# Optimization experiments

Measured on AMD Instinct MI355X. Metric: run time of the kernel, lower is better.

## Reference

```python
import jax, jax.numpy as jnp
import numpy as np

B, N, D, H = 8, 1024, 1024, 16
HD = D // H  # head_size = 64


def setup_inputs() -> dict:
    key = jax.random.key(0)
    k0, k1, k2, k3, k4 = jax.random.split(key, 5)
    scale = 1.0 / np.sqrt(D)
    return {
        "x": jax.random.normal(k0, (B, N, D), dtype=jnp.float32),
        "Wqkv": jax.random.normal(k1, (D, 3 * D), dtype=jnp.float32) * scale,
        "bqkv": jnp.zeros((3 * D,), dtype=jnp.float32),
        "Wo": jax.random.normal(k2, (D, D), dtype=jnp.float32) * scale,
        "bo": jnp.zeros((D,), dtype=jnp.float32),
    }


def reference(x, Wqkv, bqkv, Wo, bo):
    # Fused QKV projection: [B, N, 3D]
    qkv = jnp.einsum("bnd,de->bne", x, Wqkv) + bqkv
    q, k, v = jnp.split(qkv, 3, axis=-1)

    def split_heads(t):  # [B, N, D] -> [B, H, N, HD]
        return t.reshape(B, N, H, HD).transpose(0, 2, 1, 3)

    q, k, v = split_heads(q), split_heads(k), split_heads(v)

    # Scaled dot-product attention (no mask, dropout=0)
    scores = jnp.einsum("bhqd,bhkd->bhqk", q, k) / jnp.sqrt(jnp.float32(HD))
    alpha = jax.nn.softmax(scores, axis=-1)
    ctx = jnp.einsum("bhqk,bhkd->bhqd", alpha, v)  # [B, H, N, HD]

    ctx = ctx.transpose(0, 2, 1, 3).reshape(B, N, D)
    out = jnp.einsum("bnd,de->bne", ctx, Wo) + bo
    return out
```

## Files before the change

kernel.cpp:

```cpp
#include <hip/hip_runtime.h>
#include <cstdint>
#include <cstddef>

typedef _Float16 half_t;
typedef __attribute__((ext_vector_type(4))) _Float16 half4v;
typedef __attribute__((ext_vector_type(8))) _Float16 half8v;
typedef __attribute__((ext_vector_type(4))) float float4v;
typedef __attribute__((ext_vector_type(16))) float float16v;
typedef __attribute__((ext_vector_type(4))) unsigned uint4v;
typedef __attribute__((ext_vector_type(2))) int int2v;

typedef __attribute__((address_space(1))) const void gv_t;
typedef __attribute__((address_space(3))) void lv_t;

__device__ __forceinline__ void lds_cp16(const void* g, void* l) {
  __builtin_amdgcn_global_load_lds((gv_t*)g, (lv_t*)l, 16, 0, 0);
}

__device__ __forceinline__ unsigned pkh(float a, float b) {
  return __builtin_bit_cast(unsigned, __builtin_amdgcn_cvt_pkrtz(a, b));
}

__global__ __launch_bounds__(256) void k_cvt(const float* __restrict__ in,
                                             half_t* __restrict__ out) {
  int i = blockIdx.x * 256 + threadIdx.x;
  float4 v = ((const float4*)in)[i];
  half4v h = {(half_t)v.x, (half_t)v.y, (half_t)v.z, (half_t)v.w};
  ((half4v*)out)[i] = h;
}

__global__ __launch_bounds__(256) void k_tcvt(const float* __restrict__ in,
                                              half_t* __restrict__ out, int R, int C) {
  __shared__ float t[32][33];
  int c0 = blockIdx.x * 32, r0 = blockIdx.y * 32;
  int tc = threadIdx.x & 31, tr = threadIdx.x >> 5;
#pragma unroll
  for (int i = 0; i < 4; i++)
    t[tr + i * 8][tc] = in[(size_t)(r0 + tr + i * 8) * C + c0 + tc];
  __syncthreads();
#pragma unroll
  for (int i = 0; i < 4; i++)
    out[(size_t)(c0 + tr + i * 8) * R + r0 + tc] = (half_t)t[tc][tr + i * 8];
}

template <int EPI>
__global__ __launch_bounds__(256) void k_gemm(
    const half_t* __restrict__ A, const half_t* __restrict__ Bt,
    const float* __restrict__ bias, float* __restrict__ Cout,
    half_t* __restrict__ Qo, half_t* __restrict__ Ko, half_t* __restrict__ Vo,
    int M, int N, int K) {
  __shared__ half_t As[2][128 * 32];
  __shared__ half_t Bs[2][128 * 32];
  const int tid = threadIdx.x;
  const int lane = tid & 63;
  const int w = tid >> 6;
  const int xcd = blockIdx.x & 7;
  const int l = blockIdx.x >> 3;
  const int nc = l >> 6, r = l & 63;
  const int m0 = (xcd * 8 + (r >> 3)) * 128;
  const int n0 = (nc * 8 + (r & 7)) * 128;
  const int wr = w >> 1, wc = w & 1;

  const int c0 = w * 2, c1 = c0 + 1;
  const int srow = lane >> 2;
  const int sr0 = c0 * 16 + srow;
  const int sr1 = c1 * 16 + srow;
  const int scol = ((lane & 3) ^ ((lane >> 3) & 3)) * 8;

  const half_t* Ag0 = A + (size_t)(m0 + sr0) * K + scol;
  const half_t* Ag1 = A + (size_t)(m0 + sr1) * K + scol;
  const half_t* Bg0 = Bt + (size_t)(n0 + sr0) * K + scol;
  const half_t* Bg1 = Bt + (size_t)(n0 + sr1) * K + scol;

  float4v acc[4][4] = {};

  const int fr = lane & 15;
  const int fg = lane >> 4;
  const int cswz = (fg ^ ((fr >> 1) & 3)) * 8;
  const int aoff = (wr * 64 + fr) * 32 + cswz;
  const int boff = (wc * 64 + fr) * 32 + cswz;

  lds_cp16(Ag0, &As[0][c0 * 512]);
  lds_cp16(Ag1, &As[0][c1 * 512]);
  lds_cp16(Bg0, &Bs[0][c0 * 512]);
  lds_cp16(Bg1, &Bs[0][c1 * 512]);
  __syncthreads();

  const int NT = K >> 5;
  int cur = 0;
  for (int t = 0; t < NT; t++) {
    if (t + 1 < NT) {
      const int kn = (t + 1) * 32;
      lds_cp16(Ag0 + kn, &As[cur ^ 1][c0 * 512]);
      lds_cp16(Ag1 + kn, &As[cur ^ 1][c1 * 512]);
      lds_cp16(Bg0 + kn, &Bs[cur ^ 1][c0 * 512]);
      lds_cp16(Bg1 + kn, &Bs[cur ^ 1][c1 * 512]);
    }
    half8v a[4], b[4];
#pragma unroll
    for (int m = 0; m < 4; m++) a[m] = *(const half8v*)(&As[cur][aoff + m * 512]);
#pragma unroll
    for (int n = 0; n < 4; n++) b[n] = *(const half8v*)(&Bs[cur][boff + n * 512]);
#pragma unroll
    for (int m = 0; m < 4; m++)
#pragma unroll
      for (int n = 0; n < 4; n++)
        acc[m][n] = __builtin_amdgcn_mfma_f32_16x16x32_f16(a[m], b[n], acc[m][n], 0, 0, 0);
    __syncthreads();
    cur ^= 1;
  }

  const int rq = (lane >> 4) * 4;
  const int cc = lane & 15;
  if constexpr (EPI == 0) {
#pragma unroll
    for (int n = 0; n < 4; n++) {
      int e = n0 + wc * 64 + n * 16 + cc;
      float bv = bias[e];
      int which = e >> 10, h = (e >> 6) & 15, hd = e & 63;
#pragma unroll
      for (int m = 0; m < 4; m++) {
        int rowb = m0 + wr * 64 + m * 16 + rq;
#pragma unroll
        for (int r2 = 0; r2 < 4; r2++) {
          int row = rowb + r2;
          int b_ = row >> 10, tok = row & 1023;
          half_t hv = (half_t)(acc[m][n][r2] + bv);
          size_t bh = (size_t)(b_ * 16 + h);
          if (which == 0)
            Qo[(bh * 1024 + tok) * 64 + hd] = hv;
          else if (which == 1)
            Ko[(bh * 1024 + tok) * 64 + hd] = hv;
          else
            Vo[(bh * 64 + hd) * 1024 + tok] = hv;
        }
      }
    }
  } else {
#pragma unroll
    for (int n = 0; n < 4; n++) {
      int e = n0 + wc * 64 + n * 16 + cc;
      float bv = bias[e];
#pragma unroll
      for (int m = 0; m < 4; m++) {
        int rowb = m0 + wr * 64 + m * 16 + rq;
#pragma unroll
        for (int r2 = 0; r2 < 4; r2++)
          Cout[(size_t)(rowb + r2) * N + e] = acc[m][n][r2] + bv;
      }
    }
  }
}

__global__ __launch_bounds__(512, 4) void k_attn(const half_t* __restrict__ Qh,
                                                 const half_t* __restrict__ Kh,
                                                 const half_t* __restrict__ Vt,
                                                 half_t* __restrict__ ctx) {
  __shared__ alignas(16) half_t Ks[2][64 * 64];
  __shared__ alignas(16) half_t Vs[2][64 * 64];
  const int lane = threadIdx.x & 63;
  const int w = threadIdx.x >> 6;
  const int ql = lane & 31, hi = lane >> 5;
  const int xcd = blockIdx.x & 7, loc = blockIdx.x >> 3;
  const int bh = xcd * 16 + (loc >> 2), qb = loc & 3;
  const int b_ = bh >> 4, h = bh & 15;
  const int q0 = qb * 256 + w * 32;

  const half_t* Qp = Qh + (size_t)bh * (1024 * 64);
  const half_t* Kp = Kh + (size_t)bh * (1024 * 64);
  const half_t* Vp = Vt + (size_t)bh * (64 * 1024);

  half8v qf[4];
#pragma unroll
  for (int c = 0; c < 4; c++) {
    half8v tq = *(const half8v*)(Qp + (size_t)(q0 + ql) * 64 + c * 16 + hi * 8);
    qf[c] = tq * (_Float16)0.125f;
  }

  const int G = w * 64 + lane;
  const int rS = G >> 3;
  const int gS = (G & 7) ^ (rS & 7);

  float16v co[2] = {};
  float mr = -1e30f, ssum = 0.f;

  lds_cp16(Kp + (size_t)rS * 64 + gS * 8, &Ks[0][w * 512]);
  lds_cp16(Vp + (size_t)rS * 1024 + 0 + gS * 8, &Vs[0][w * 512]);
  __syncthreads();

  int cur = 0;
  for (int t = 0; t < 16; t++) {
    if (t < 15) {
      const int kn = (t + 1) * 64;
      lds_cp16(Kp + (size_t)(kn + rS) * 64 + gS * 8, &Ks[cur ^ 1][w * 512]);
      lds_cp16(Vp + (size_t)rS * 1024 + kn + gS * 8, &Vs[cur ^ 1][w * 512]);
    }

    float16v sacc[2] = {};
    __builtin_amdgcn_s_setprio(1);
#pragma unroll
    for (int c = 0; c < 4; c++)
#pragma unroll
      for (int s = 0; s < 2; s++) {
        int row = s * 32 + ql;
        half8v kf = *(const half8v*)(&Ks[cur][row * 64 + (((2 * c + hi) ^ (row & 7)) * 8)]);
        sacc[s] = __builtin_amdgcn_mfma_f32_32x32x16_f16(kf, qf[c], sacc[s], 0, 0, 0);
      }
    __builtin_amdgcn_s_setprio(0);

    float mx = -1e30f;
#pragma unroll
    for (int s = 0; s < 2; s++)
#pragma unroll
      for (int i = 0; i < 16; i++) mx = fmaxf(mx, sacc[s][i]);
    mx = fmaxf(mx, __shfl_xor(mx, 32, 64));
    if (mx > mr + 8.f) {
      float fac = __expf(mr - mx);
      mr = mx;
      ssum *= fac;
#pragma unroll
      for (int dd = 0; dd < 2; dd++)
#pragma unroll
        for (int i = 0; i < 16; i++) co[dd][i] *= fac;
    }
    float rsum = 0.f;
#pragma unroll
    for (int s = 0; s < 2; s++)
#pragma unroll
      for (int i = 0; i < 16; i++) {
        float e = __expf(sacc[s][i] - mr);
        sacc[s][i] = e;
        rsum += e;
      }
    rsum += __shfl_xor(rsum, 32, 64);
    ssum += rsum;

#pragma unroll
    for (int kc = 0; kc < 4; kc++) {
      const int s = kc >> 1, o = (kc & 1) * 8;
      unsigned dA0 = pkh(sacc[s][o + 0], sacc[s][o + 1]);
      unsigned dA1 = pkh(sacc[s][o + 2], sacc[s][o + 3]);
      unsigned dB0 = pkh(sacc[s][o + 4], sacc[s][o + 5]);
      unsigned dB1 = pkh(sacc[s][o + 6], sacc[s][o + 7]);
      int2v r0 = __builtin_amdgcn_permlane32_swap((int)dA0, (int)dB0, false, false);
      int2v r1 = __builtin_amdgcn_permlane32_swap((int)dA1, (int)dB1, false, false);
      uint4v pw = {(unsigned)r0.x, (unsigned)r1.x, (unsigned)r0.y, (unsigned)r1.y};
      half8v pf = __builtin_bit_cast(half8v, pw);
      __builtin_amdgcn_s_setprio(1);
#pragma unroll
      for (int dd = 0; dd < 2; dd++) {
        int row = dd * 32 + ql;
        half8v vf = *(const half8v*)(&Vs[cur][row * 64 + (((2 * kc + hi) ^ (row & 7)) * 8)]);
        co[dd] = __builtin_amdgcn_mfma_f32_32x32x16_f16(vf, pf, co[dd], 0, 0, 0);
      }
      __builtin_amdgcn_s_setprio(0);
    }
    __syncthreads();
    cur ^= 1;
  }

  float rinv = 1.0f / ssum;
  half_t* outp = ctx + ((size_t)(b_ * 1024 + q0 + ql) * 1024 + h * 64);
#pragma unroll
  for (int dd = 0; dd < 2; dd++)
#pragma unroll
    for (int g = 0; g < 4; g++) {
      int d0 = dd * 32 + g * 8 + hi * 4;
      unsigned p0 = pkh(co[dd][g * 4 + 0] * rinv, co[dd][g * 4 + 1] * rinv);
      unsigned p1 = pkh(co[dd][g * 4 + 2] * rinv, co[dd][g * 4 + 3] * rinv);
      *(unsigned*)(outp + d0) = p0;
      *(unsigned*)(outp + d0 + 2) = p1;
    }
}

extern "C" void kernel_launch(void* const* d_in, const int* in_sizes, int n_in,
                              void* d_out, int out_size, void* d_ws, size_t ws_size,
                              hipStream_t stream) {
  const float* x = (const float*)d_in[0];
  const float* Wqkv = (const float*)d_in[1];
  const float* bqkv = (const float*)d_in[2];
  const float* Wo = (const float*)d_in[3];
  const float* bo = (const float*)d_in[4];
  float* out = (float*)d_out;
  char* ws = (char*)d_ws;

  const size_t NEED = 75497472;
  if (ws_size < NEED) return;
  half_t* xh = (half_t*)(ws);
  half_t* wqkvT = (half_t*)(ws + 16777216);
  half_t* woT = (half_t*)(ws + 23068672);
  half_t* Qh = (half_t*)(ws + 25165824);
  half_t* Kh = (half_t*)(ws + 41943040);
  half_t* Vt = (half_t*)(ws + 58720256);
  half_t* ctxh = xh;

  k_cvt<<<8192, 256, 0, stream>>>(x, xh);
  k_tcvt<<<dim3(96, 32), 256, 0, stream>>>(Wqkv, wqkvT, 1024, 3072);
  k_tcvt<<<dim3(32, 32), 256, 0, stream>>>(Wo, woT, 1024, 1024);
  k_gemm<0><<<1536, 256, 0, stream>>>(xh, wqkvT, bqkv, nullptr, Qh, Kh, Vt,
                                      8192, 3072, 1024);
  k_attn<<<512, 512, 0, stream>>>(Qh, Kh, Vt, ctxh);
  k_gemm<1><<<512, 256, 0, stream>>>(ctxh, woT, bo, out, nullptr, nullptr, nullptr,
                                     8192, 1024, 1024);
}
```

Measured before the change: 178.6 us.

## Use 256x256 tiled 8-wave QKV GEMM with deeper K tiles and interleaved prefetch

Replaces the templated QKV projection GEMM with a dedicated kernel using 256x256 block tiles, 512 threads, BK=64 and XOR-swizzled LDS. Global-to-LDS prefetch of the next K tile is issued inside the compute sub-steps, with barriers and s_setprio around the MFMA bursts. The larger tile raises operand reuse and cuts global traffic, but uses 128KB of LDS per block and more registers, and leaves only 384 blocks, which limits occupancy. The output GEMM is split into its own non-templated kernel with unchanged behavior.

```diff
diff --git a/kernel.cpp b/kernel.cpp
--- a/kernel.cpp
+++ b/kernel.cpp
@@ -43,12 +43,125 @@
     out[(size_t)(c0 + tr + i * 8) * R + r0 + tc] = (half_t)t[tc][tr + i * 8];
 }
 
-template <int EPI>
-__global__ __launch_bounds__(256) void k_gemm(
+__global__ __launch_bounds__(512, 2) void k_gemm_qkv(
     const half_t* __restrict__ A, const half_t* __restrict__ Bt,
-    const float* __restrict__ bias, float* __restrict__ Cout,
-    half_t* __restrict__ Qo, half_t* __restrict__ Ko, half_t* __restrict__ Vo,
-    int M, int N, int K) {
+    const float* __restrict__ bias,
+    half_t* __restrict__ Qo, half_t* __restrict__ Ko, half_t* __restrict__ Vo) {
+  __shared__ half_t As[2][256 * 64];
+  __shared__ half_t Bs[2][256 * 64];
+  const int tid = threadIdx.x;
+  const int lane = tid & 63;
+  const int w = tid >> 6;
+  const int wr = w >> 2, wc = w & 3;
+  const int fr = lane & 15, fg = lane >> 4;
+
+  const int bid = blockIdx.x;
+  const int xcd = bid & 7, l = bid >> 3;
+  const int mi = xcd * 4 + ((l >> 2) & 3);
+  const int ni = (l >> 4) * 4 + (l & 3);
+  const int m0 = mi * 256, n0 = ni * 256;
+
+  const half_t* sp[8];
+  int dof[8];
+#pragma unroll
+  for (int q = 0; q < 8; ++q) {
+    const int hh = q >> 1, j = q & 1;
+    const int G = j * 512 + tid;
+    const int r = G >> 3, sg = G & 7;
+    const int gg = sg ^ (r & 7);
+    dof[q] = (hh & 1) * 8192 + G * 8;
+    if (hh < 2)
+      sp[q] = A + (size_t)(m0 + hh * 128 + r) * 1024 + gg * 8;
+    else
+      sp[q] = Bt + (size_t)(n0 + (hh - 2) * 128 + r) * 1024 + gg * 8;
+  }
+
+  float4v acc[8][4] = {};
+  half8v bq[4][2];
+
+#pragma unroll
+  for (int q = 0; q < 8; ++q)
+    lds_cp16(sp[q], (q < 4 ? &As[0][0] : &Bs[0][0]) + dof[q]);
+  asm volatile("s_waitcnt vmcnt(0)" ::: "memory");
+  __builtin_amdgcn_s_barrier();
+
+  for (int kt = 0; kt < 16; ++kt) {
+    const int cb = kt & 1, nb = cb ^ 1;
+#pragma unroll
+    for (int mq = 0; mq < 4; ++mq) {
+      half8v av[2][2];
+#pragma unroll
+      for (int mp = 0; mp < 2; ++mp)
+#pragma unroll
+        for (int kk = 0; kk < 2; ++kk) {
+          const int row = wr * 128 + (mq * 2 + mp) * 16 + fr;
+          av[mp][kk] =
+              *(const half8v*)(&As[cb][row * 64 + ((((kk << 2) | fg) ^ (fr & 7)) * 8)]);
+        }
+      if (mq == 0) {
+#pragma unroll
+        for (int n = 0; n < 4; ++n)
+#pragma unroll
+          for (int kk = 0; kk < 2; ++kk) {
+            const int row = wc * 64 + n * 16 + fr;
+            bq[n][kk] =
+                *(const half8v*)(&Bs[cb][row * 64 + ((((kk << 2) | fg) ^ (fr & 7)) * 8)]);
+          }
+        if (kt < 15) {
+          const int koff = (kt + 1) * 64;
+#pragma unroll
+          for (int q = 0; q < 8; ++q)
+            lds_cp16(sp[q] + koff, (q < 4 ? &As[nb][0] : &Bs[nb][0]) + dof[q]);
+        }
+      }
+      __builtin_amdgcn_s_barrier();
+      asm volatile("s_waitcnt lgkmcnt(0)" ::: "memory");
+      __builtin_amdgcn_sched_barrier(0);
+      __builtin_amdgcn_s_setprio(1);
+#pragma unroll
+      for (int kk = 0; kk < 2; ++kk)
+#pragma unroll
+        for (int mp = 0; mp < 2; ++mp)
+#pragma unroll
+          for (int n = 0; n < 4; ++n)
+            acc[mq * 2 + mp][n] = __builtin_amdgcn_mfma_f32_16x16x32_f16(
+                av[mp][kk], bq[n][kk], acc[mq * 2 + mp][n], 0, 0, 0);
+      __builtin_amdgcn_s_setprio(0);
+      if (mq == 3) asm volatile("s_waitcnt vmcnt(0)" ::: "memory");
+      __builtin_amdgcn_s_barrier();
+    }
+  }
+
+  const int rq = (lane >> 4) * 4;
+  const int cc = lane & 15;
+#pragma unroll
+  for (int n = 0; n < 4; ++n) {
+    const int e = n0 + wc * 64 + n * 16 + cc;
+    const float bv = bias[e];
+    const int which = e >> 10, h = (e >> 6) & 15, hd = e & 63;
+#pragma unroll
+    for (int m = 0; m < 8; ++m) {
+      const int rowb = m0 + wr * 128 + m * 16 + rq;
+#pragma unroll
+      for (int r2 = 0; r2 < 4; ++r2) {
+        const int row = rowb + r2;
+        const int b_ = row >> 10, tok = row & 1023;
+        const half_t hv = (half_t)(acc[m][n][r2] + bv);
+        const size_t bh = (size_t)(b_ * 16 + h);
+        if (which == 0)
+          Qo[(bh * 1024 + tok) * 64 + hd] = hv;
+        else if (which == 1)
+          Ko[(bh * 1024 + tok) * 64 + hd] = hv;
+        else
+          Vo[(bh * 64 + hd) * 1024 + tok] = hv;
+      }
+    }
+  }
+}
+
+__global__ __launch_bounds__(256) void k_gemm_o(
+    const half_t* __restrict__ A, const half_t* __restrict__ Bt,
+    const float* __restrict__ bias, float* __restrict__ Cout, int N, int K) {
   __shared__ half_t As[2][128 * 32];
   __shared__ half_t Bs[2][128 * 32];
   const int tid = threadIdx.x;
@@ -112,42 +225,16 @@
 
   const int rq = (lane >> 4) * 4;
   const int cc = lane & 15;
-  if constexpr (EPI == 0) {
-#pragma unroll
-    for (int n = 0; n < 4; n++) {
-      int e = n0 + wc * 64 + n * 16 + cc;
-      float bv = bias[e];
-      int which = e >> 10, h = (e >> 6) & 15, hd = e & 63;
-#pragma unroll
-      for (int m = 0; m < 4; m++) {
-        int rowb = m0 + wr * 64 + m * 16 + rq;
-#pragma unroll
-        for (int r2 = 0; r2 < 4; r2++) {
-          int row = rowb + r2;
-          int b_ = row >> 10, tok = row & 1023;
-          half_t hv = (half_t)(acc[m][n][r2] + bv);
-          size_t bh = (size_t)(b_ * 16 + h);
-          if (which == 0)
-            Qo[(bh * 1024 + tok) * 64 + hd] = hv;
-          else if (which == 1)
-            Ko[(bh * 1024 + tok) * 64 + hd] = hv;
-          else
-            Vo[(bh * 64 + hd) * 1024 + tok] = hv;
-        }
-      }
-    }
-  } else {
-#pragma unroll
-    for (int n = 0; n < 4; n++) {
-      int e = n0 + wc * 64 + n * 16 + cc;
-      float bv = bias[e];
-#pragma unroll
-      for (int m = 0; m < 4; m++) {
-        int rowb = m0 + wr * 64 + m * 16 + rq;
-#pragma unroll
-        for (int r2 = 0; r2 < 4; r2++)
-          Cout[(size_t)(rowb + r2) * N + e] = acc[m][n][r2] + bv;
-      }
+#pragma unroll
+  for (int n = 0; n < 4; n++) {
+    int e = n0 + wc * 64 + n * 16 + cc;
+    float bv = bias[e];
+#pragma unroll
+    for (int m = 0; m < 4; m++) {
+      int rowb = m0 + wr * 64 + m * 16 + rq;
+#pragma unroll
+      for (int r2 = 0; r2 < 4; r2++)
+        Cout[(size_t)(rowb + r2) * N + e] = acc[m][n][r2] + bv;
     }
   }
 }
@@ -297,9 +384,7 @@
   k_cvt<<<8192, 256, 0, stream>>>(x, xh);
   k_tcvt<<<dim3(96, 32), 256, 0, stream>>>(Wqkv, wqkvT, 1024, 3072);
   k_tcvt<<<dim3(32, 32), 256, 0, stream>>>(Wo, woT, 1024, 1024);
-  k_gemm<0><<<1536, 256, 0, stream>>>(xh, wqkvT, bqkv, nullptr, Qh, Kh, Vt,
-                                      8192, 3072, 1024);
+  k_gemm_qkv<<<384, 512, 0, stream>>>(xh, wqkvT, bqkv, Qh, Kh, Vt);
   k_attn<<<512, 512, 0, stream>>>(Qh, Kh, Vt, ctxh);
-  k_gemm<1><<<512, 256, 0, stream>>>(ctxh, woT, bo, out, nullptr, nullptr, nullptr,
-                                     8192, 1024, 1024);
-}
+  k_gemm_o<<<512, 256, 0, stream>>>(ctxh, woT, bo, out, 1024, 1024);
+}
```

New measurement: 199.6 us. +11.8%, slower.

## Deepen GEMM LDS pipeline to four buffers with prefetch distance two

Applied to the files above, without the earlier changes.

The GEMM main loop moves from a double-buffered LDS scheme to a four-slot ring that prefetches two K-tiles ahead. A manual vmcnt wait plus a single barrier per iteration replaces the trailing __syncthreads, so more global-to-LDS loads can be in flight while MFMAs run. It also raises wave priority around the MFMA block. LDS use doubles to 64 KB per block, which may lower occupancy, and correctness depends on the hand-chosen vmcnt counts.

```diff
diff --git a/kernel.cpp b/kernel.cpp
--- a/kernel.cpp
+++ b/kernel.cpp
@@ -49,8 +49,8 @@
     const float* __restrict__ bias, float* __restrict__ Cout,
     half_t* __restrict__ Qo, half_t* __restrict__ Ko, half_t* __restrict__ Vo,
     int M, int N, int K) {
-  __shared__ half_t As[2][128 * 32];
-  __shared__ half_t Bs[2][128 * 32];
+  __shared__ half_t As[4][128 * 32];
+  __shared__ half_t Bs[4][128 * 32];
   const int tid = threadIdx.x;
   const int lane = tid & 63;
   const int w = tid >> 6;
@@ -80,34 +80,47 @@
   const int aoff = (wr * 64 + fr) * 32 + cswz;
   const int boff = (wc * 64 + fr) * 32 + cswz;
 
-  lds_cp16(Ag0, &As[0][c0 * 512]);
-  lds_cp16(Ag1, &As[0][c1 * 512]);
-  lds_cp16(Bg0, &Bs[0][c0 * 512]);
-  lds_cp16(Bg1, &Bs[0][c1 * 512]);
-  __syncthreads();
-
   const int NT = K >> 5;
-  int cur = 0;
+#pragma unroll
+  for (int p = 0; p < 2; ++p) {
+    const int kn = p * 32;
+    lds_cp16(Ag0 + kn, &As[p][c0 * 512]);
+    lds_cp16(Ag1 + kn, &As[p][c1 * 512]);
+    lds_cp16(Bg0 + kn, &Bs[p][c0 * 512]);
+    lds_cp16(Bg1 + kn, &Bs[p][c1 * 512]);
+  }
+
   for (int t = 0; t < NT; t++) {
-    if (t + 1 < NT) {
-      const int kn = (t + 1) * 32;
-      lds_cp16(Ag0 + kn, &As[cur ^ 1][c0 * 512]);
-      lds_cp16(Ag1 + kn, &As[cur ^ 1][c1 * 512]);
-      lds_cp16(Bg0 + kn, &Bs[cur ^ 1][c0 * 512]);
-      lds_cp16(Bg1 + kn, &Bs[cur ^ 1][c1 * 512]);
-    }
+    if (t + 2 < NT) {
+      const int nb = (t + 2) & 3;
+      const int kn = (t + 2) * 32;
+      lds_cp16(Ag0 + kn, &As[nb][c0 * 512]);
+      lds_cp16(Ag1 + kn, &As[nb][c1 * 512]);
+      lds_cp16(Bg0 + kn, &Bs[nb][c0 * 512]);
+      lds_cp16(Bg1 + kn, &Bs[nb][c1 * 512]);
+    }
+    if (t + 2 < NT)
+      asm volatile("s_waitcnt vmcnt(8)" ::: "memory");
+    else if (t + 1 < NT)
+      asm volatile("s_waitcnt vmcnt(4)" ::: "memory");
+    else
+      asm volatile("s_waitcnt vmcnt(0)" ::: "memory");
+    __builtin_amdgcn_s_barrier();
+    __builtin_amdgcn_sched_barrier(0);
+
+    const int cb = t & 3;
     half8v a[4], b[4];
 #pragma unroll
-    for (int m = 0; m < 4; m++) a[m] = *(const half8v*)(&As[cur][aoff + m * 512]);
-#pragma unroll
-    for (int n = 0; n < 4; n++) b[n] = *(const half8v*)(&Bs[cur][boff + n * 512]);
+    for (int m = 0; m < 4; m++) a[m] = *(const half8v*)(&As[cb][aoff + m * 512]);
+#pragma unroll
+    for (int n = 0; n < 4; n++) b[n] = *(const half8v*)(&Bs[cb][boff + n * 512]);
+    __builtin_amdgcn_s_setprio(1);
 #pragma unroll
     for (int m = 0; m < 4; m++)
 #pragma unroll
       for (int n = 0; n < 4; n++)
         acc[m][n] = __builtin_amdgcn_mfma_f32_16x16x32_f16(a[m], b[n], acc[m][n], 0, 0, 0);
-    __syncthreads();
-    cur ^= 1;
+    __builtin_amdgcn_s_setprio(0);
   }
 
   const int rq = (lane >> 4) * 4;
```

Result: no change. 176.6 us (-1.1%).
